# Performance work log

Measured on AMD Instinct MI355X. Metric: run time of the kernel, lower is better.

Reference implementation:

```python
import jax, jax.numpy as jnp
import numpy as np

B, S, D = 4, 1024, 1024   # batch, seq_len, d_model (isize=hsize=osize)
H, AD = 16, 64            # num_head, attn_dim = hsize // num_head
K_REL = 16                # k_rel_pos (bidirectional: 2*K+1 = 33 embeddings)
EPS = 1e-8                # SparseNormer eps (ieps_default)


def setup_inputs() -> dict:
    key = jax.random.key(0)
    ks = jax.random.split(key, 5)
    scale = 0.02
    return {
        "iQ": jax.random.normal(ks[0], (B, S, D), jnp.float32),
        "Wa": jax.random.normal(ks[1], (3 * D, D), jnp.float32) * scale,   # adaptor weight
        "ba": jnp.zeros((3 * D,), jnp.float32),                            # adaptor bias
        "rel_emb": jax.random.normal(ks[2], (2 * K_REL + 1, AD), jnp.float32) * scale,
        "sn_bias": jnp.zeros((1,), jnp.float32),                           # SparseNormer bias
        "Wo": jax.random.normal(ks[3], (D, D), jnp.float32) * scale,       # outer weight
        "bo": jnp.zeros((D,), jnp.float32),                                # outer bias
    }


def reference(iQ, Wa, ba, rel_emb, sn_bias, Wo, bo):
    b, s, _ = iQ.shape
    # fused QKV projection: [B,S,3*H*AD] -> q,k,v each [B,H,S,AD]
    qkv = (iQ @ Wa.T + ba).reshape(b, s, 3, H, AD)
    q = qkv[:, :, 0].transpose(0, 2, 1, 3)
    k = qkv[:, :, 1].transpose(0, 2, 1, 3)
    v = qkv[:, :, 2].transpose(0, 2, 1, 3)

    # content scores [B,H,S,S]
    scores = jnp.einsum('bhqd,bhkd->bhqk', q, k)

    # relative-position term: rel_pos[i,j] = clip(j-i, -K, K) + K
    pos = jnp.arange(s)
    rp = jnp.clip(pos[None, :] - pos[:, None], -K_REL, K_REL) + K_REL  # [S,S] int
    r = rel_emb[rp]                                                     # [S,S,AD]
    scores = scores + jnp.einsum('bhqd,qkd->bhqk', q, r)

    scores = scores / jnp.sqrt(jnp.asarray(AD, scores.dtype))

    # SparseNormer: relu(x + b)^2 / (sum + eps)
    t = jax.nn.relu(scores + sn_bias)
    t = t * t
    attn = t / (t.sum(-1, keepdims=True) + EPS)

    ctx = jnp.einsum('bhqk,bhkd->bhqd', attn, v)          # [B,H,S,AD]
    ctx = ctx.transpose(0, 2, 1, 3).reshape(b, s, H * AD)  # [B,S,hsize]
    return ctx @ Wo.T + bo
```

## Files before the change

kernel.cpp:

```cpp
#include <hip/hip_runtime.h>
#include <hip/hip_bf16.h>
#include <stdint.h>

typedef unsigned short u16;
typedef unsigned int   u32;
typedef __attribute__((ext_vector_type(8))) __bf16 bf16x8;
typedef __attribute__((ext_vector_type(4))) float  f32x4;
typedef __attribute__((ext_vector_type(2))) u32    u32x2;

#define B_  4
#define S_  1024
#define D_  1024
#define H_  16
#define AD_ 64

#if defined(__has_builtin)
#if __has_builtin(__builtin_amdgcn_cvt_pk_bf16_f32)
#define HAVE_CVT_PK 1
#endif
#if __has_builtin(__builtin_amdgcn_global_load_lds)
#define HAVE_GLL 1
#endif
#endif

#ifdef HAVE_CVT_PK
typedef __attribute__((ext_vector_type(2))) __bf16 bf16x2;
__device__ __forceinline__ u32 pack2(float a, float b) {
    bf16x2 r = __builtin_amdgcn_cvt_pk_bf16_f32(a, b);
    return __builtin_bit_cast(u32, r);
}
__device__ __forceinline__ u16 f2bf(float f) {
    return (u16)pack2(f, f);
}
#else
__device__ __forceinline__ u16 f2bf(float f) {
    u32 u = __float_as_uint(f);
    u32 r = u + 0x7fffu + ((u >> 16) & 1u);
    return (u16)(r >> 16);
}
__device__ __forceinline__ u32 pack2(float a, float b) {
    return (u32)f2bf(a) | ((u32)f2bf(b) << 16);
}
#endif

typedef __attribute__((address_space(1))) const u32 gas_u32;
typedef __attribute__((address_space(3))) u32 las_u32;
__device__ __forceinline__ void gll16(const void* g, void* l) {
#ifdef HAVE_GLL
    __builtin_amdgcn_global_load_lds((gas_u32*)g, (las_u32*)l, 16, 0, 0);
#else
    int lane = threadIdx.x & 63;
    *(uint4*)((u16*)l + lane * 8) = *(const uint4*)g;
#endif
}

__global__ __launch_bounds__(256) void conv_bf16(
    const float* __restrict__ a, const float* __restrict__ b,
    const float* __restrict__ c,
    u16* __restrict__ ao, u16* __restrict__ bo, u16* __restrict__ co,
    int na, int nb)
{
    int gid = blockIdx.x * 256 + threadIdx.x;
    int base = gid * 8;
    const float* src; u16* dst; int off;
    if (base < na)           { src = a; dst = ao; off = base; }
    else if (base < na + nb) { src = b; dst = bo; off = base - na; }
    else                     { src = c; dst = co; off = base - na - nb; }
    float4 v0 = *(const float4*)(src + off);
    float4 v1 = *(const float4*)(src + off + 4);
    u32 pk[4] = {pack2(v0.x, v0.y), pack2(v0.z, v0.w),
                 pack2(v1.x, v1.y), pack2(v1.z, v1.w)};
    *(uint4*)(dst + off) = *(uint4*)pk;
}

__global__ __launch_bounds__(256) void qkv_gemm(
    const u16* __restrict__ A, const u16* __restrict__ W,
    const float* __restrict__ bias,
    u16* __restrict__ qb, u16* __restrict__ kb, u16* __restrict__ vb)
{
    __shared__ u16 As[128 * 64];
    __shared__ u16 Bs[128 * 64];

    const int tid  = threadIdx.x;
    const int lane = tid & 63, w = tid >> 6;
    const int quad = lane >> 4, ln = lane & 15;
    const int wrow = (w >> 1) * 64, wcol = (w & 1) * 64;
    const int row0 = blockIdx.y * 128, col0 = blockIdx.x * 128;

    const int ri = lane >> 3, ci = lane & 7;
    const int scol = (ci ^ ri) << 3;

    f32x4 acc[4][4];
#pragma unroll
    for (int i = 0; i < 4; i++)
#pragma unroll
        for (int j = 0; j < 4; j++) acc[i][j] = (f32x4){0.f, 0.f, 0.f, 0.f};

    for (int kb_i = 0; kb_i < 16; ++kb_i) {
        const int k0 = kb_i * 64;
#pragma unroll
        for (int c = 0; c < 4; ++c) {
            int r0 = c * 32 + w * 8;
            int gr = r0 + ri;
            gll16(A + (size_t)(row0 + gr) * D_ + k0 + scol, &As[r0 * 64]);
            gll16(W + (size_t)(col0 + gr) * D_ + k0 + scol, &Bs[r0 * 64]);
        }
        __syncthreads();
#pragma unroll
        for (int ks = 0; ks < 2; ++ks) {
            bf16x8 af[4], bfr[4];
#pragma unroll
            for (int mt = 0; mt < 4; ++mt) {
                int r = wrow + mt * 16 + ln;
                af[mt] = *(bf16x8*)&As[r * 64 + (((ks * 4 + quad) ^ (r & 7)) << 3)];
            }
#pragma unroll
            for (int nt = 0; nt < 4; ++nt) {
                int r = wcol + nt * 16 + ln;
                bfr[nt] = *(bf16x8*)&Bs[r * 64 + (((ks * 4 + quad) ^ (r & 7)) << 3)];
            }
#pragma unroll
            for (int mt = 0; mt < 4; ++mt)
#pragma unroll
                for (int nt = 0; nt < 4; ++nt)
                    acc[mt][nt] = __builtin_amdgcn_mfma_f32_16x16x32_bf16(
                        af[mt], bfr[nt], acc[mt][nt], 0, 0, 0);
        }
        __syncthreads();
    }

    const int which = col0 >> 10;
#pragma unroll
    for (int mt = 0; mt < 4; ++mt) {
#pragma unroll
        for (int nt = 0; nt < 4; ++nt) {
            int n = col0 + wcol + nt * 16 + ln;
            float bv = bias[n];
            int h = (n >> 6) & 15, d = n & 63;
            if (which == 2) {
                int m0 = row0 + wrow + mt * 16 + quad * 4;
                int b = m0 >> 10, s0 = m0 & 1023;
                u32x2 pk;
                pk.x = pack2(acc[mt][nt][0] + bv, acc[mt][nt][1] + bv);
                pk.y = pack2(acc[mt][nt][2] + bv, acc[mt][nt][3] + bv);
                *(u32x2*)&vb[((size_t)((b * 16 + h) * 64 + d)) * 1024 + s0] = pk;
            } else {
#pragma unroll
                for (int reg = 0; reg < 4; ++reg) {
                    int m = row0 + wrow + mt * 16 + quad * 4 + reg;
                    int b = m >> 10, s = m & 1023;
                    float v = acc[mt][nt][reg] + bv;
                    if (which == 0)
                        qb[((size_t)((b * 16 + h) * 1024 + s)) * 64 + d] = f2bf(v * 0.125f);
                    else
                        kb[((size_t)((b * 16 + h) * 1024 + s)) * 64 + d] = f2bf(v);
                }
            }
        }
    }
}

__global__ __launch_bounds__(256) void attn_kernel(
    const u16* __restrict__ qb, const u16* __restrict__ kb,
    const u16* __restrict__ vb, const float* __restrict__ rel,
    const float* __restrict__ snb_p, u16* __restrict__ ctx)
{
    __shared__ u16 q_s[64 * 64];
    __shared__ u16 k_s[64 * 64];
    __shared__ u16 v_s[64 * 64];
    __shared__ u16 t_s[64 * 64];
    __shared__ float qr[33 * 64];

    u16* rel_s = t_s;

    const int tid  = threadIdx.x;
    const int lane = tid & 63, w = tid >> 6;
    const int quad = lane >> 4, ln = lane & 15;
    const int strip = w * 16;
    const int bh = blockIdx.x >> 4, qt = blockIdx.x & 15;
    const int i0 = qt * 64;
    const float snb = snb_p[0];

    const u16* qplane = qb + ((size_t)bh * 1024 + i0) * 64;
    const u16* kplane = kb + (size_t)bh * 1024 * 64;
    const u16* vplane = vb + (size_t)bh * 64 * 1024;

    const int ri = lane >> 3, ci = lane & 7;
    const int scol = (ci ^ ri) << 3;

#pragma unroll
    for (int c = 0; c < 2; ++c) {
        int r0 = w * 16 + c * 8;
        int gr = r0 + ri;
        gll16(qplane + (size_t)gr * 64 + scol, &q_s[r0 * 64]);
    }
    for (int idx = tid; idx < 384; idx += 256) {
        int p = idx >> 3, c = idx & 7;
        u32 pk[4];
        if (p < 33) {
            const float* sp = rel + p * 64 + c * 8;
            float4 r0 = *(const float4*)sp;
            float4 r1 = *(const float4*)(sp + 4);
            pk[0] = pack2(r0.x, r0.y); pk[1] = pack2(r0.z, r0.w);
            pk[2] = pack2(r1.x, r1.y); pk[3] = pack2(r1.z, r1.w);
        } else { pk[0] = pk[1] = pk[2] = pk[3] = 0; }
        *(uint4*)&rel_s[p * 64 + ((c ^ (p & 7)) << 3)] = *(uint4*)pk;
    }
    __syncthreads();

    {
        f32x4 qacc[3];
#pragma unroll
        for (int nt = 0; nt < 3; ++nt) qacc[nt] = (f32x4){0.f, 0.f, 0.f, 0.f};
#pragma unroll
        for (int ks = 0; ks < 2; ++ks) {
            int rq = strip + ln;
            bf16x8 aq = *(bf16x8*)&q_s[rq * 64 + (((ks * 4 + quad) ^ (rq & 7)) << 3)];
#pragma unroll
            for (int nt = 0; nt < 3; ++nt) {
                int rp = nt * 16 + ln;
                bf16x8 bp = *(bf16x8*)&rel_s[rp * 64 + (((ks * 4 + quad) ^ (rp & 7)) << 3)];
                qacc[nt] = __builtin_amdgcn_mfma_f32_16x16x32_bf16(aq, bp, qacc[nt], 0, 0, 0);
            }
        }
#pragma unroll
        for (int nt = 0; nt < 3; ++nt) {
            int p = nt * 16 + ln;
            if (p < 33) {
#pragma unroll
                for (int reg = 0; reg < 4; ++reg)
                    qr[p * 64 + strip + quad * 4 + reg] = qacc[nt][reg];
            }
        }
    }
    __syncthreads();

    const int iloc = strip + ln;
    const float cL = qr[iloc] + snb;
    const float cR = qr[32 * 64 + iloc] + snb;

    bf16x8 bq[2];
#pragma unroll
    for (int ks = 0; ks < 2; ++ks)
        bq[ks] = *(bf16x8*)&q_s[iloc * 64 + (((ks * 4 + quad) ^ (iloc & 7)) << 3)];

    float Lsum = 0.f;
    f32x4 o_acc[4];
#pragma unroll
    for (int nt = 0; nt < 4; ++nt) o_acc[nt] = (f32x4){0.f, 0.f, 0.f, 0.f};

    for (int jt = 0; jt < 16; ++jt) {
        const int j0 = jt * 64;
        __syncthreads();
#pragma unroll
        for (int c = 0; c < 2; ++c) {
            int r0 = w * 16 + c * 8;
            int gr = r0 + ri;
            gll16(kplane + (size_t)(j0 + gr) * 64 + scol, &k_s[r0 * 64]);
            gll16(vplane + (size_t)gr * 1024 + j0 + scol, &v_s[r0 * 64]);
        }
        __syncthreads();

        f32x4 sacc[4];
#pragma unroll
        for (int mj = 0; mj < 4; ++mj) sacc[mj] = (f32x4){0.f, 0.f, 0.f, 0.f};
#pragma unroll
        for (int ks = 0; ks < 2; ++ks) {
#pragma unroll
            for (int mj = 0; mj < 4; ++mj) {
                int rk = mj * 16 + ln;
                bf16x8 ak = *(bf16x8*)&k_s[rk * 64 + (((ks * 4 + quad) ^ (rk & 7)) << 3)];
                sacc[mj] = __builtin_amdgcn_mfma_f32_16x16x32_bf16(ak, bq[ks], sacc[mj], 0, 0, 0);
            }
        }

        const int d0 = j0 - i0;
        if (d0 <= -128 || d0 >= 128) {
            const float c = (d0 < 0) ? cL : cR;
#pragma unroll
            for (int mj = 0; mj < 4; ++mj) {
                float tv[4];
#pragma unroll
                for (int reg = 0; reg < 4; ++reg) {
                    float t = fmaxf(sacc[mj][reg] + c, 0.f);
                    t = t * t;
                    Lsum += t;
                    tv[reg] = t;
                }
                u32x2 pk;
                pk.x = pack2(tv[0], tv[1]);
                pk.y = pack2(tv[2], tv[3]);
                int jl = mj * 16 + quad * 4;
                int chunk = (jl >> 3) ^ (iloc & 7);
                *(u32x2*)&t_s[iloc * 64 + (chunk << 3) + (quad & 1) * 4] = pk;
            }
        } else {
#pragma unroll
            for (int mj = 0; mj < 4; ++mj) {
                int jbase = j0 + mj * 16 + quad * 4;
                float tv[4];
#pragma unroll
                for (int reg = 0; reg < 4; ++reg) {
                    int dlt = jbase + reg - (i0 + iloc);
                    int p = min(max(dlt, -16), 16) + 16;
                    float t = fmaxf(sacc[mj][reg] + qr[p * 64 + iloc] + snb, 0.f);
                    t = t * t;
                    Lsum += t;
                    tv[reg] = t;
                }
                u32x2 pk;
                pk.x = pack2(tv[0], tv[1]);
                pk.y = pack2(tv[2], tv[3]);
                int jl = mj * 16 + quad * 4;
                int chunk = (jl >> 3) ^ (iloc & 7);
                *(u32x2*)&t_s[iloc * 64 + (chunk << 3) + (quad & 1) * 4] = pk;
            }
        }

#pragma unroll
        for (int ks = 0; ks < 2; ++ks) {
            bf16x8 at = *(bf16x8*)&t_s[iloc * 64 + (((ks * 4 + quad) ^ (iloc & 7)) << 3)];
#pragma unroll
            for (int nt = 0; nt < 4; ++nt) {
                int rv = nt * 16 + ln;
                bf16x8 bv = *(bf16x8*)&v_s[rv * 64 + (((ks * 4 + quad) ^ (rv & 7)) << 3)];
                o_acc[nt] = __builtin_amdgcn_mfma_f32_16x16x32_bf16(at, bv, o_acc[nt], 0, 0, 0);
            }
        }
    }

    Lsum += __shfl_xor(Lsum, 16);
    Lsum += __shfl_xor(Lsum, 32);
    float Linv = 1.f / (Lsum + 1e-8f);

    const int b = bh >> 4, h = bh & 15;
#pragma unroll
    for (int reg = 0; reg < 4; ++reg) {
        int ig = i0 + strip + quad * 4 + reg;
        float li = __shfl(Linv, quad * 4 + reg);
#pragma unroll
        for (int nt = 0; nt < 4; ++nt) {
            int dg = nt * 16 + ln;
            ctx[((size_t)(b * 1024 + ig)) * 1024 + h * 64 + dg] =
                f2bf(o_acc[nt][reg] * li);
        }
    }
}

__global__ __launch_bounds__(256) void out_gemm(
    const u16* __restrict__ A, const u16* __restrict__ W,
    const float* __restrict__ bias, float* __restrict__ out)
{
    __shared__ u16 As[128 * 64];
    __shared__ u16 Bs[128 * 64];

    const int tid  = threadIdx.x;
    const int lane = tid & 63, w = tid >> 6;
    const int quad = lane >> 4, ln = lane & 15;
    const int wrow = (w >> 1) * 64, wcol = (w & 1) * 64;
    const int row0 = blockIdx.y * 128, col0 = blockIdx.x * 128;

    const int ri = lane >> 3, ci = lane & 7;
    const int scol = (ci ^ ri) << 3;

    f32x4 acc[4][4];
#pragma unroll
    for (int i = 0; i < 4; i++)
#pragma unroll
        for (int j = 0; j < 4; j++) acc[i][j] = (f32x4){0.f, 0.f, 0.f, 0.f};

    for (int kb_i = 0; kb_i < 16; ++kb_i) {
        const int k0 = kb_i * 64;
#pragma unroll
        for (int c = 0; c < 4; ++c) {
            int r0 = c * 32 + w * 8;
            int gr = r0 + ri;
            gll16(A + (size_t)(row0 + gr) * D_ + k0 + scol, &As[r0 * 64]);
            gll16(W + (size_t)(col0 + gr) * D_ + k0 + scol, &Bs[r0 * 64]);
        }
        __syncthreads();
#pragma unroll
        for (int ks = 0; ks < 2; ++ks) {
            bf16x8 af[4], bfr[4];
#pragma unroll
            for (int mt = 0; mt < 4; ++mt) {
                int r = wrow + mt * 16 + ln;
                af[mt] = *(bf16x8*)&As[r * 64 + (((ks * 4 + quad) ^ (r & 7)) << 3)];
            }
#pragma unroll
            for (int nt = 0; nt < 4; ++nt) {
                int r = wcol + nt * 16 + ln;
                bfr[nt] = *(bf16x8*)&Bs[r * 64 + (((ks * 4 + quad) ^ (r & 7)) << 3)];
            }
#pragma unroll
            for (int mt = 0; mt < 4; ++mt)
#pragma unroll
                for (int nt = 0; nt < 4; ++nt)
                    acc[mt][nt] = __builtin_amdgcn_mfma_f32_16x16x32_bf16(
                        af[mt], bfr[nt], acc[mt][nt], 0, 0, 0);
        }
        __syncthreads();
    }
#pragma unroll
    for (int mt = 0; mt < 4; ++mt) {
#pragma unroll
        for (int nt = 0; nt < 4; ++nt) {
            int n = col0 + wcol + nt * 16 + ln;
            float bv = bias[n];
#pragma unroll
            for (int reg = 0; reg < 4; ++reg) {
                int m = row0 + wrow + mt * 16 + quad * 4 + reg;
                out[(size_t)m * D_ + n] = acc[mt][nt][reg] + bv;
            }
        }
    }
}

extern "C" void kernel_launch(void* const* d_in, const int* in_sizes, int n_in,
                              void* d_out, int out_size, void* d_ws, size_t ws_size,
                              hipStream_t stream)
{
    const float* iQ  = (const float*)d_in[0];
    const float* Wa  = (const float*)d_in[1];
    const float* ba  = (const float*)d_in[2];
    const float* rel = (const float*)d_in[3];
    const float* snb = (const float*)d_in[4];
    const float* Wo  = (const float*)d_in[5];
    const float* bo  = (const float*)d_in[6];
    float* out = (float*)d_out;

    const size_t NQ = (size_t)B_ * S_ * D_;
    const size_t NWA = (size_t)3 * D_ * D_;
    const size_t NWO = (size_t)D_ * D_;
    const size_t PLANE = (size_t)B_ * H_ * S_ * AD_;

    u16* iQbf = (u16*)d_ws;
    u16* Wabf = iQbf + NQ;
    u16* Wobf = Wabf + NWA;
    u16* qbuf = Wobf + NWO;
    u16* kbuf = qbuf + PLANE;
    u16* vbuf = kbuf + PLANE;
    u16* ctx  = iQbf;

    conv_bf16<<<4096, 256, 0, stream>>>(iQ, Wa, Wo, iQbf, Wabf, Wobf,
                                        (int)NQ, (int)NWA);
    qkv_gemm<<<dim3(24, 32), 256, 0, stream>>>(iQbf, Wabf, ba, qbuf, kbuf, vbuf);
    attn_kernel<<<dim3(1024), 256, 0, stream>>>(qbuf, kbuf, vbuf, rel, snb, ctx);
    out_gemm<<<dim3(8, 32), 256, 0, stream>>>(ctx, Wobf, bo, out);
}
```

Baseline: 196.7 us.

## Fuse fp32-to-bf16 conversion into GEMMs, double-buffer attention with 128-row query tiles

Drops the separate conversion kernel: both GEMMs now read fp32 inputs and weights and pack them to bf16 while staging into shared memory, which removes a full read/write pass over iQ and the weights. The attention kernel handles 128 query rows per block, so each K/V tile is reused by twice as many rows, and it double-buffers K/V loads with one barrier per tile. The out GEMM uses 128x64 tiles to launch more blocks. The trade-off is that GEMM loads now go through registers and fp32 global reads are twice as wide, and the weights get reconverted by every block that reads them.

```diff
diff --git a/kernel.cpp b/kernel.cpp
--- a/kernel.cpp
+++ b/kernel.cpp
@@ -54,27 +54,8 @@
 #endif
 }
 
-__global__ __launch_bounds__(256) void conv_bf16(
-    const float* __restrict__ a, const float* __restrict__ b,
-    const float* __restrict__ c,
-    u16* __restrict__ ao, u16* __restrict__ bo, u16* __restrict__ co,
-    int na, int nb)
-{
-    int gid = blockIdx.x * 256 + threadIdx.x;
-    int base = gid * 8;
-    const float* src; u16* dst; int off;
-    if (base < na)           { src = a; dst = ao; off = base; }
-    else if (base < na + nb) { src = b; dst = bo; off = base - na; }
-    else                     { src = c; dst = co; off = base - na - nb; }
-    float4 v0 = *(const float4*)(src + off);
-    float4 v1 = *(const float4*)(src + off + 4);
-    u32 pk[4] = {pack2(v0.x, v0.y), pack2(v0.z, v0.w),
-                 pack2(v1.x, v1.y), pack2(v1.z, v1.w)};
-    *(uint4*)(dst + off) = *(uint4*)pk;
-}
-
 __global__ __launch_bounds__(256) void qkv_gemm(
-    const u16* __restrict__ A, const u16* __restrict__ W,
+    const float* __restrict__ A, const float* __restrict__ W,
     const float* __restrict__ bias,
     u16* __restrict__ qb, u16* __restrict__ kb, u16* __restrict__ vb)
 {
@@ -87,23 +68,33 @@
     const int wrow = (w >> 1) * 64, wcol = (w & 1) * 64;
     const int row0 = blockIdx.y * 128, col0 = blockIdx.x * 128;
 
-    const int ri = lane >> 3, ci = lane & 7;
-    const int scol = (ci ^ ri) << 3;
-
     f32x4 acc[4][4];
 #pragma unroll
     for (int i = 0; i < 4; i++)
 #pragma unroll
         for (int j = 0; j < 4; j++) acc[i][j] = (f32x4){0.f, 0.f, 0.f, 0.f};
+
+    const int cr = tid >> 3;
+    const int cc = tid & 7;
 
     for (int kb_i = 0; kb_i < 16; ++kb_i) {
         const int k0 = kb_i * 64;
 #pragma unroll
-        for (int c = 0; c < 4; ++c) {
-            int r0 = c * 32 + w * 8;
-            int gr = r0 + ri;
-            gll16(A + (size_t)(row0 + gr) * D_ + k0 + scol, &As[r0 * 64]);
-            gll16(W + (size_t)(col0 + gr) * D_ + k0 + scol, &Bs[r0 * 64]);
+        for (int rep = 0; rep < 4; ++rep) {
+            int r = cr + rep * 32;
+            const float* sa = A + (size_t)(row0 + r) * D_ + k0 + cc * 8;
+            const float* sb = W + (size_t)(col0 + r) * D_ + k0 + cc * 8;
+            float4 a0 = *(const float4*)sa;
+            float4 a1 = *(const float4*)(sa + 4);
+            float4 b0 = *(const float4*)sb;
+            float4 b1 = *(const float4*)(sb + 4);
+            u32 pa[4] = {pack2(a0.x, a0.y), pack2(a0.z, a0.w),
+                         pack2(a1.x, a1.y), pack2(a1.z, a1.w)};
+            u32 pb[4] = {pack2(b0.x, b0.y), pack2(b0.z, b0.w),
+                         pack2(b1.x, b1.y), pack2(b1.z, b1.w)};
+            int c = cc ^ (r & 7);
+            *(uint4*)&As[r * 64 + c * 8] = *(uint4*)pa;
+            *(uint4*)&Bs[r * 64 + c * 8] = *(uint4*)pb;
         }
         __syncthreads();
 #pragma unroll
@@ -165,20 +156,19 @@
     const u16* __restrict__ vb, const float* __restrict__ rel,
     const float* __restrict__ snb_p, u16* __restrict__ ctx)
 {
-    __shared__ u16 q_s[64 * 64];
-    __shared__ u16 k_s[64 * 64];
-    __shared__ u16 v_s[64 * 64];
-    __shared__ u16 t_s[64 * 64];
-    __shared__ float qr[33 * 64];
-
-    u16* rel_s = t_s;
+    __shared__ u16 q_s[128 * 64];
+    __shared__ u16 k_s[2][64 * 64];
+    __shared__ u16 v_s[2][64 * 64];
+    __shared__ float qr[33 * 128];
+
+    u16* t_s   = q_s;
+    u16* rel_s = v_s[1];
 
     const int tid  = threadIdx.x;
     const int lane = tid & 63, w = tid >> 6;
     const int quad = lane >> 4, ln = lane & 15;
-    const int strip = w * 16;
-    const int bh = blockIdx.x >> 4, qt = blockIdx.x & 15;
-    const int i0 = qt * 64;
+    const int bh = blockIdx.x >> 3, qt = blockIdx.x & 7;
+    const int i0 = qt * 128;
     const float snb = snb_p[0];
 
     const u16* qplane = qb + ((size_t)bh * 1024 + i0) * 64;
@@ -189,10 +179,9 @@
     const int scol = (ci ^ ri) << 3;
 
 #pragma unroll
-    for (int c = 0; c < 2; ++c) {
-        int r0 = w * 16 + c * 8;
-        int gr = r0 + ri;
-        gll16(qplane + (size_t)gr * 64 + scol, &q_s[r0 * 64]);
+    for (int c = 0; c < 4; ++c) {
+        int r0 = w * 32 + c * 8;
+        gll16(qplane + (size_t)(r0 + ri) * 64 + scol, &q_s[r0 * 64]);
     }
     for (int idx = tid; idx < 384; idx += 256) {
         int p = idx >> 3, c = idx & 7;
@@ -208,19 +197,27 @@
     }
     __syncthreads();
 
-    {
+    bf16x8 bq[2][2];
+#pragma unroll
+    for (int sub = 0; sub < 2; ++sub) {
+        int rq = w * 32 + sub * 16 + ln;
+#pragma unroll
+        for (int ks = 0; ks < 2; ++ks)
+            bq[sub][ks] = *(bf16x8*)&q_s[rq * 64 + (((ks * 4 + quad) ^ (rq & 7)) << 3)];
+    }
+
+#pragma unroll
+    for (int sub = 0; sub < 2; ++sub) {
         f32x4 qacc[3];
 #pragma unroll
         for (int nt = 0; nt < 3; ++nt) qacc[nt] = (f32x4){0.f, 0.f, 0.f, 0.f};
 #pragma unroll
         for (int ks = 0; ks < 2; ++ks) {
-            int rq = strip + ln;
-            bf16x8 aq = *(bf16x8*)&q_s[rq * 64 + (((ks * 4 + quad) ^ (rq & 7)) << 3)];
 #pragma unroll
             for (int nt = 0; nt < 3; ++nt) {
                 int rp = nt * 16 + ln;
                 bf16x8 bp = *(bf16x8*)&rel_s[rp * 64 + (((ks * 4 + quad) ^ (rp & 7)) << 3)];
-                qacc[nt] = __builtin_amdgcn_mfma_f32_16x16x32_bf16(aq, bp, qacc[nt], 0, 0, 0);
+                qacc[nt] = __builtin_amdgcn_mfma_f32_16x16x32_bf16(bq[sub][ks], bp, qacc[nt], 0, 0, 0);
             }
         }
 #pragma unroll
@@ -229,173 +226,198 @@
             if (p < 33) {
 #pragma unroll
                 for (int reg = 0; reg < 4; ++reg)
-                    qr[p * 64 + strip + quad * 4 + reg] = qacc[nt][reg];
-            }
-        }
+                    qr[p * 128 + w * 32 + sub * 16 + quad * 4 + reg] = qacc[nt][reg];
+            }
+        }
+    }
+
+#pragma unroll
+    for (int c = 0; c < 2; ++c) {
+        int r0 = w * 16 + c * 8;
+        gll16(kplane + (size_t)(r0 + ri) * 64 + scol, &k_s[0][r0 * 64]);
+        gll16(vplane + (size_t)(r0 + ri) * 1024 + scol, &v_s[0][r0 * 64]);
     }
     __syncthreads();
 
-    const int iloc = strip + ln;
-    const float cL = qr[iloc] + snb;
-    const float cR = qr[32 * 64 + iloc] + snb;
-
-    bf16x8 bq[2];
-#pragma unroll
-    for (int ks = 0; ks < 2; ++ks)
-        bq[ks] = *(bf16x8*)&q_s[iloc * 64 + (((ks * 4 + quad) ^ (iloc & 7)) << 3)];
-
-    float Lsum = 0.f;
-    f32x4 o_acc[4];
-#pragma unroll
-    for (int nt = 0; nt < 4; ++nt) o_acc[nt] = (f32x4){0.f, 0.f, 0.f, 0.f};
+    float cL[2], cR[2], Lsum[2] = {0.f, 0.f};
+#pragma unroll
+    for (int sub = 0; sub < 2; ++sub) {
+        int il = w * 32 + sub * 16 + ln;
+        cL[sub] = qr[il] + snb;
+        cR[sub] = qr[32 * 128 + il] + snb;
+    }
+
+    f32x4 o_acc[2][4];
+#pragma unroll
+    for (int sub = 0; sub < 2; ++sub)
+#pragma unroll
+        for (int nt = 0; nt < 4; ++nt) o_acc[sub][nt] = (f32x4){0.f, 0.f, 0.f, 0.f};
 
     for (int jt = 0; jt < 16; ++jt) {
+        const int cur = jt & 1;
         const int j0 = jt * 64;
-        __syncthreads();
-#pragma unroll
-        for (int c = 0; c < 2; ++c) {
-            int r0 = w * 16 + c * 8;
-            int gr = r0 + ri;
-            gll16(kplane + (size_t)(j0 + gr) * 64 + scol, &k_s[r0 * 64]);
-            gll16(vplane + (size_t)gr * 1024 + j0 + scol, &v_s[r0 * 64]);
-        }
-        __syncthreads();
-
-        f32x4 sacc[4];
-#pragma unroll
-        for (int mj = 0; mj < 4; ++mj) sacc[mj] = (f32x4){0.f, 0.f, 0.f, 0.f};
+        if (jt < 15) {
+            const int nxt = 1 - cur;
+#pragma unroll
+            for (int c = 0; c < 2; ++c) {
+                int r0 = w * 16 + c * 8;
+                gll16(kplane + (size_t)(j0 + 64 + r0 + ri) * 64 + scol, &k_s[nxt][r0 * 64]);
+                gll16(vplane + (size_t)(r0 + ri) * 1024 + (j0 + 64) + scol, &v_s[nxt][r0 * 64]);
+            }
+        }
+
+        f32x4 sacc[2][4];
+#pragma unroll
+        for (int sub = 0; sub < 2; ++sub)
+#pragma unroll
+            for (int mj = 0; mj < 4; ++mj) sacc[sub][mj] = (f32x4){0.f, 0.f, 0.f, 0.f};
 #pragma unroll
         for (int ks = 0; ks < 2; ++ks) {
 #pragma unroll
             for (int mj = 0; mj < 4; ++mj) {
                 int rk = mj * 16 + ln;
-                bf16x8 ak = *(bf16x8*)&k_s[rk * 64 + (((ks * 4 + quad) ^ (rk & 7)) << 3)];
-                sacc[mj] = __builtin_amdgcn_mfma_f32_16x16x32_bf16(ak, bq[ks], sacc[mj], 0, 0, 0);
-            }
-        }
-
-        const int d0 = j0 - i0;
-        if (d0 <= -128 || d0 >= 128) {
-            const float c = (d0 < 0) ? cL : cR;
+                bf16x8 ak = *(bf16x8*)&k_s[cur][rk * 64 + (((ks * 4 + quad) ^ (rk & 7)) << 3)];
+                sacc[0][mj] = __builtin_amdgcn_mfma_f32_16x16x32_bf16(ak, bq[0][ks], sacc[0][mj], 0, 0, 0);
+                sacc[1][mj] = __builtin_amdgcn_mfma_f32_16x16x32_bf16(ak, bq[1][ks], sacc[1][mj], 0, 0, 0);
+            }
+        }
+
+#pragma unroll
+        for (int sub = 0; sub < 2; ++sub) {
+            const int ib = i0 + w * 32 + sub * 16;
+            const int row = w * 32 + sub * 16 + ln;
 #pragma unroll
             for (int mj = 0; mj < 4; ++mj) {
+                const int jg0 = j0 + mj * 16;
+                const int diff = jg0 - ib;
                 float tv[4];
-#pragma unroll
-                for (int reg = 0; reg < 4; ++reg) {
-                    float t = fmaxf(sacc[mj][reg] + c, 0.f);
-                    t = t * t;
-                    Lsum += t;
-                    tv[reg] = t;
+                if (diff >= 32 || diff <= -32) {
+                    const float c = (diff < 0) ? cL[sub] : cR[sub];
+#pragma unroll
+                    for (int reg = 0; reg < 4; ++reg) {
+                        float t = fmaxf(sacc[sub][mj][reg] + c, 0.f);
+                        t = t * t;
+                        Lsum[sub] += t;
+                        tv[reg] = t;
+                    }
+                } else {
+#pragma unroll
+                    for (int reg = 0; reg < 4; ++reg) {
+                        int dlt = jg0 + quad * 4 + reg - (ib + ln);
+                        int p = min(max(dlt, -16), 16) + 16;
+                        float t = fmaxf(sacc[sub][mj][reg] + qr[p * 128 + row] + snb, 0.f);
+                        t = t * t;
+                        Lsum[sub] += t;
+                        tv[reg] = t;
+                    }
                 }
                 u32x2 pk;
                 pk.x = pack2(tv[0], tv[1]);
                 pk.y = pack2(tv[2], tv[3]);
-                int jl = mj * 16 + quad * 4;
-                int chunk = (jl >> 3) ^ (iloc & 7);
-                *(u32x2*)&t_s[iloc * 64 + (chunk << 3) + (quad & 1) * 4] = pk;
-            }
-        } else {
-#pragma unroll
-            for (int mj = 0; mj < 4; ++mj) {
-                int jbase = j0 + mj * 16 + quad * 4;
-                float tv[4];
-#pragma unroll
-                for (int reg = 0; reg < 4; ++reg) {
-                    int dlt = jbase + reg - (i0 + iloc);
-                    int p = min(max(dlt, -16), 16) + 16;
-                    float t = fmaxf(sacc[mj][reg] + qr[p * 64 + iloc] + snb, 0.f);
-                    t = t * t;
-                    Lsum += t;
-                    tv[reg] = t;
-                }
-                u32x2 pk;
-                pk.x = pack2(tv[0], tv[1]);
-                pk.y = pack2(tv[2], tv[3]);
-                int jl = mj * 16 + quad * 4;
-                int chunk = (jl >> 3) ^ (iloc & 7);
-                *(u32x2*)&t_s[iloc * 64 + (chunk << 3) + (quad & 1) * 4] = pk;
+                int chunk = ((2 * mj + (quad >> 1)) ^ (row & 7));
+                *(u32x2*)&t_s[row * 64 + (chunk << 3) + (quad & 1) * 4] = pk;
             }
         }
 
 #pragma unroll
         for (int ks = 0; ks < 2; ++ks) {
-            bf16x8 at = *(bf16x8*)&t_s[iloc * 64 + (((ks * 4 + quad) ^ (iloc & 7)) << 3)];
+            bf16x8 at[2];
+#pragma unroll
+            for (int sub = 0; sub < 2; ++sub) {
+                int rt = w * 32 + sub * 16 + ln;
+                at[sub] = *(bf16x8*)&t_s[rt * 64 + (((ks * 4 + quad) ^ (rt & 7)) << 3)];
+            }
 #pragma unroll
             for (int nt = 0; nt < 4; ++nt) {
                 int rv = nt * 16 + ln;
-                bf16x8 bv = *(bf16x8*)&v_s[rv * 64 + (((ks * 4 + quad) ^ (rv & 7)) << 3)];
-                o_acc[nt] = __builtin_amdgcn_mfma_f32_16x16x32_bf16(at, bv, o_acc[nt], 0, 0, 0);
-            }
-        }
-    }
-
-    Lsum += __shfl_xor(Lsum, 16);
-    Lsum += __shfl_xor(Lsum, 32);
-    float Linv = 1.f / (Lsum + 1e-8f);
+                bf16x8 bv = *(bf16x8*)&v_s[cur][rv * 64 + (((ks * 4 + quad) ^ (rv & 7)) << 3)];
+                o_acc[0][nt] = __builtin_amdgcn_mfma_f32_16x16x32_bf16(at[0], bv, o_acc[0][nt], 0, 0, 0);
+                o_acc[1][nt] = __builtin_amdgcn_mfma_f32_16x16x32_bf16(at[1], bv, o_acc[1][nt], 0, 0, 0);
+            }
+        }
+        __syncthreads();
+    }
 
     const int b = bh >> 4, h = bh & 15;
 #pragma unroll
-    for (int reg = 0; reg < 4; ++reg) {
-        int ig = i0 + strip + quad * 4 + reg;
-        float li = __shfl(Linv, quad * 4 + reg);
-#pragma unroll
-        for (int nt = 0; nt < 4; ++nt) {
-            int dg = nt * 16 + ln;
-            ctx[((size_t)(b * 1024 + ig)) * 1024 + h * 64 + dg] =
-                f2bf(o_acc[nt][reg] * li);
+    for (int sub = 0; sub < 2; ++sub) {
+        float ls = Lsum[sub];
+        ls += __shfl_xor(ls, 16);
+        ls += __shfl_xor(ls, 32);
+        float Linv = 1.f / (ls + 1e-8f);
+#pragma unroll
+        for (int reg = 0; reg < 4; ++reg) {
+            int ig = i0 + w * 32 + sub * 16 + quad * 4 + reg;
+            float li = __shfl(Linv, quad * 4 + reg);
+#pragma unroll
+            for (int nt = 0; nt < 4; ++nt) {
+                int dg = nt * 16 + ln;
+                ctx[((size_t)(b * 1024 + ig)) * 1024 + h * 64 + dg] =
+                    f2bf(o_acc[sub][nt][reg] * li);
+            }
         }
     }
 }
 
 __global__ __launch_bounds__(256) void out_gemm(
-    const u16* __restrict__ A, const u16* __restrict__ W,
+    const u16* __restrict__ A, const float* __restrict__ W,
     const float* __restrict__ bias, float* __restrict__ out)
 {
     __shared__ u16 As[128 * 64];
-    __shared__ u16 Bs[128 * 64];
+    __shared__ u16 Bs[64 * 64];
 
     const int tid  = threadIdx.x;
     const int lane = tid & 63, w = tid >> 6;
     const int quad = lane >> 4, ln = lane & 15;
-    const int wrow = (w >> 1) * 64, wcol = (w & 1) * 64;
-    const int row0 = blockIdx.y * 128, col0 = blockIdx.x * 128;
+    const int wrow = (w >> 1) * 64, wcol = (w & 1) * 32;
+    const int row0 = blockIdx.y * 128, col0 = blockIdx.x * 64;
 
     const int ri = lane >> 3, ci = lane & 7;
     const int scol = (ci ^ ri) << 3;
-
-    f32x4 acc[4][4];
+    const int cr = tid >> 3, cc = tid & 7;
+
+    f32x4 acc[4][2];
 #pragma unroll
     for (int i = 0; i < 4; i++)
 #pragma unroll
-        for (int j = 0; j < 4; j++) acc[i][j] = (f32x4){0.f, 0.f, 0.f, 0.f};
+        for (int j = 0; j < 2; j++) acc[i][j] = (f32x4){0.f, 0.f, 0.f, 0.f};
 
     for (int kb_i = 0; kb_i < 16; ++kb_i) {
         const int k0 = kb_i * 64;
 #pragma unroll
         for (int c = 0; c < 4; ++c) {
             int r0 = c * 32 + w * 8;
-            int gr = r0 + ri;
-            gll16(A + (size_t)(row0 + gr) * D_ + k0 + scol, &As[r0 * 64]);
-            gll16(W + (size_t)(col0 + gr) * D_ + k0 + scol, &Bs[r0 * 64]);
+            gll16(A + (size_t)(row0 + r0 + ri) * D_ + k0 + scol, &As[r0 * 64]);
+        }
+#pragma unroll
+        for (int rep = 0; rep < 2; ++rep) {
+            int r = cr + rep * 32;
+            const float* sb = W + (size_t)(col0 + r) * D_ + k0 + cc * 8;
+            float4 b0 = *(const float4*)sb;
+            float4 b1 = *(const float4*)(sb + 4);
+            u32 pb[4] = {pack2(b0.x, b0.y), pack2(b0.z, b0.w),
+                         pack2(b1.x, b1.y), pack2(b1.z, b1.w)};
+            int c = cc ^ (r & 7);
+            *(uint4*)&Bs[r * 64 + c * 8] = *(uint4*)pb;
         }
         __syncthreads();
 #pragma unroll
         for (int ks = 0; ks < 2; ++ks) {
-            bf16x8 af[4], bfr[4];
+            bf16x8 af[4], bfr[2];
 #pragma unroll
             for (int mt = 0; mt < 4; ++mt) {
                 int r = wrow + mt * 16 + ln;
                 af[mt] = *(bf16x8*)&As[r * 64 + (((ks * 4 + quad) ^ (r & 7)) << 3)];
             }
 #pragma unroll
-            for (int nt = 0; nt < 4; ++nt) {
+            for (int nt = 0; nt < 2; ++nt) {
                 int r = wcol + nt * 16 + ln;
                 bfr[nt] = *(bf16x8*)&Bs[r * 64 + (((ks * 4 + quad) ^ (r & 7)) << 3)];
             }
 #pragma unroll
             for (int mt = 0; mt < 4; ++mt)
 #pragma unroll
-                for (int nt = 0; nt < 4; ++nt)
+                for (int nt = 0; nt < 2; ++nt)
                     acc[mt][nt] = __builtin_amdgcn_mfma_f32_16x16x32_bf16(
                         af[mt], bfr[nt], acc[mt][nt], 0, 0, 0);
         }
@@ -404,7 +426,7 @@
 #pragma unroll
     for (int mt = 0; mt < 4; ++mt) {
 #pragma unroll
-        for (int nt = 0; nt < 4; ++nt) {
+        for (int nt = 0; nt < 2; ++nt) {
             int n = col0 + wcol + nt * 16 + ln;
             float bv = bias[n];
 #pragma unroll
@@ -429,22 +451,14 @@
     const float* bo  = (const float*)d_in[6];
     float* out = (float*)d_out;
 
-    const size_t NQ = (size_t)B_ * S_ * D_;
-    const size_t NWA = (size_t)3 * D_ * D_;
-    const size_t NWO = (size_t)D_ * D_;
     const size_t PLANE = (size_t)B_ * H_ * S_ * AD_;
 
-    u16* iQbf = (u16*)d_ws;
-    u16* Wabf = iQbf + NQ;
-    u16* Wobf = Wabf + NWA;
-    u16* qbuf = Wobf + NWO;
+    u16* qbuf = (u16*)d_ws;
     u16* kbuf = qbuf + PLANE;
     u16* vbuf = kbuf + PLANE;
-    u16* ctx  = iQbf;
-
-    conv_bf16<<<4096, 256, 0, stream>>>(iQ, Wa, Wo, iQbf, Wabf, Wobf,
-                                        (int)NQ, (int)NWA);
-    qkv_gemm<<<dim3(24, 32), 256, 0, stream>>>(iQbf, Wabf, ba, qbuf, kbuf, vbuf);
-    attn_kernel<<<dim3(1024), 256, 0, stream>>>(qbuf, kbuf, vbuf, rel, snb, ctx);
-    out_gemm<<<dim3(8, 32), 256, 0, stream>>>(ctx, Wobf, bo, out);
-}
+    u16* ctx  = vbuf + PLANE;
+
+    qkv_gemm<<<dim3(24, 32), 256, 0, stream>>>(iQ, Wa, ba, qbuf, kbuf, vbuf);
+    attn_kernel<<<dim3(512), 256, 0, stream>>>(qbuf, kbuf, vbuf, rel, snb, ctx);
+    out_gemm<<<dim3(16, 32), 256, 0, stream>>>(ctx, Wo, bo, out);
+}
```

Result: slower. 261.6 us (+33.0%).
